# Performance work log

Hardware: AMD Instinct MI355X
Metric: run time of the kernel (lower is better)

## Reference

```python
import jax, jax.numpy as jnp
import numpy as np

N_NODES = 100000
N_EDGES = 1600000
IN_DIM = 512
OUT_DIM = 64


def setup_inputs() -> dict:
    key = jax.random.key(0)
    k1, k2, k3 = jax.random.split(key, 3)
    x = jax.random.normal(k1, (N_NODES, IN_DIM), dtype=jnp.float32)
    edge_index = jax.random.randint(k2, (2, N_EDGES), 0, N_NODES, dtype=jnp.int64)
    # Glorot-ish init for the GCNConv linear weight, stored as [in, out]
    W = jax.random.normal(k3, (IN_DIM, OUT_DIM), dtype=jnp.float32) * (1.0 / np.sqrt(IN_DIM))
    b = jnp.zeros((OUT_DIM,), dtype=jnp.float32)
    return {"x": x, "edge_index": edge_index, "W": W, "b": b}


def reference(x, edge_index, W, b):
    N = x.shape[0]
    # --- gcn_norm: add self-loops, symmetric degree normalization ---
    loop = jnp.arange(N, dtype=edge_index.dtype)
    src = jnp.concatenate([edge_index[0], loop])  # message sources
    dst = jnp.concatenate([edge_index[1], loop])  # aggregation targets
    deg = jax.ops.segment_sum(jnp.ones_like(dst, dtype=x.dtype), dst, num_segments=N)
    deg_inv_sqrt = jnp.where(deg > 0, jax.lax.rsqrt(jnp.maximum(deg, 1.0)), 0.0)
    norm = deg_inv_sqrt[src] * deg_inv_sqrt[dst]  # [E+N]
    # --- linear transform then gather-scale-scatter aggregation ---
    h = x @ W                                   # [N, out]
    msg = h[src] * norm[:, None]                # [E+N, out]
    out = jax.ops.segment_sum(msg, dst, num_segments=N) + b
    return jax.nn.log_softmax(out, axis=1)
```

## Files before the change

### kernel.cpp

```cpp
#include <hip/hip_runtime.h>
#include <math.h>

#define N_NODES 100000
#define N_EDGES 1600000
#define IN_DIM 512
#define OUT_DIM 64
#define NB 1024
#define NPB 128
#define CHUNK (N_EDGES / NPB)
#define N_BUCKETS_USED 782
#define N_TILES128 782
#define GEMM_BLOCKS 256

typedef __attribute__((ext_vector_type(8))) short short8;
typedef __attribute__((ext_vector_type(4))) float float4v;

__device__ __forceinline__ unsigned short f2bf(float f) {
    unsigned int u = __float_as_uint(f);
    u += 0x7fffu + ((u >> 16) & 1u);
    return (unsigned short)(u >> 16);
}
__device__ __forceinline__ float bf2f(unsigned short s) {
    return __uint_as_float(((unsigned int)s) << 16);
}
__device__ __forceinline__ short8 cvt8(float4v lo, float4v hi) {
    union { short8 s8; unsigned short us[8]; } af;
    af.us[0] = f2bf(lo.x); af.us[1] = f2bf(lo.y);
    af.us[2] = f2bf(lo.z); af.us[3] = f2bf(lo.w);
    af.us[4] = f2bf(hi.x); af.us[5] = f2bf(hi.y);
    af.us[6] = f2bf(hi.z); af.us[7] = f2bf(hi.w);
    return af.s8;
}
__device__ __forceinline__ void gload_lds16(const void* g, void* lds) {
    __builtin_amdgcn_global_load_lds(
        (const __attribute__((address_space(1))) unsigned int*)g,
        (__attribute__((address_space(3))) unsigned int*)lds, 16, 0, 0);
}

__global__ __launch_bounds__(256) void k_hist1(const int* __restrict__ dst,
                                               int* __restrict__ blockHist) {
    __shared__ int hist[NB];
    const int t = threadIdx.x, b = blockIdx.x;
    for (int k = t; k < NB; k += 256) hist[k] = 0;
    __syncthreads();
    const int e0 = b * CHUNK;
    for (int i = t; i < CHUNK; i += 256)
        atomicAdd(&hist[dst[e0 + i] >> 7], 1);
    __syncthreads();
    for (int k = t; k < NB; k += 256) blockHist[k * NPB + b] = hist[k];
}

__global__ __launch_bounds__(256) void k_offsets(const int* __restrict__ blockHist,
                                                 int* __restrict__ blockStart,
                                                 int* __restrict__ bucketBase) {
    __shared__ int colsum[NB];
    __shared__ int bbase[NB + 1];
    __shared__ int wtot[4];
    const int t = threadIdx.x, lane = t & 63, w = t >> 6;
    for (int k = t; k < NB; k += 256) {
        const int4* p = (const int4*)(blockHist + k * NPB);
        int s = 0;
#pragma unroll
        for (int j = 0; j < NPB / 4; ++j) {
            int4 v = p[j];
            s += v.x + v.y + v.z + v.w;
        }
        colsum[k] = s;
    }
    __syncthreads();
    int c0 = colsum[t * 4 + 0], c1 = colsum[t * 4 + 1];
    int c2 = colsum[t * 4 + 2], c3 = colsum[t * 4 + 3];
    int tsum = c0 + c1 + c2 + c3;
    int incl = tsum;
#pragma unroll
    for (int off = 1; off < 64; off <<= 1) {
        int u = __shfl_up(incl, off, 64);
        if (lane >= off) incl += u;
    }
    if (lane == 63) wtot[w] = incl;
    __syncthreads();
    int woff = 0;
#pragma unroll
    for (int k2 = 0; k2 < 4; ++k2) if (k2 < w) woff += wtot[k2];
    int excl = woff + incl - tsum;
    bbase[t * 4 + 0] = excl;
    bbase[t * 4 + 1] = excl + c0;
    bbase[t * 4 + 2] = excl + c0 + c1;
    bbase[t * 4 + 3] = excl + c0 + c1 + c2;
    if (t == 255) bbase[NB] = excl + tsum;
    __syncthreads();
    for (int k = t; k < NB + 1; k += 256) bucketBase[k] = bbase[k];
    for (int k = t; k < NB; k += 256) {
        int run = bbase[k];
        const int* ph = blockHist + k * NPB;
        int* ps = blockStart + k * NPB;
        for (int b = 0; b < NPB; ++b) {
            ps[b] = run;
            run += ph[b];
        }
    }
}

__global__ __launch_bounds__(256) void k_partition(const int* __restrict__ dst,
                                                   const int* __restrict__ src,
                                                   const int* __restrict__ blockStart,
                                                   int* __restrict__ parts) {
    __shared__ int cursor[NB];
    const int t = threadIdx.x, b = blockIdx.x;
    for (int k = t; k < NB; k += 256) cursor[k] = blockStart[k * NPB + b];
    __syncthreads();
    const int e0 = b * CHUNK;
    for (int i = t; i < CHUNK; i += 256) {
        int d = dst[e0 + i];
        int s = src[e0 + i];
        int k = d >> 7;
        int pos = atomicAdd(&cursor[k], 1);
        parts[pos] = ((d & 127) << 17) | s;
    }
}

__global__ __launch_bounds__(256) void k_bucket(const int* __restrict__ parts,
                                                const int* __restrict__ bucketBase,
                                                int* __restrict__ degi,
                                                int* __restrict__ row_ptr,
                                                int* __restrict__ csr) {
    __shared__ int cnt[128];
    __shared__ int cur[128];
    __shared__ int wtot[2];
    const int t = threadIdx.x, k = blockIdx.x;
    const int base = bucketBase[k];
    const int n    = bucketBase[k + 1] - base;
    if (t < 128) cnt[t] = 0;
    __syncthreads();
    for (int i = t; i < n; i += 256)
        atomicAdd(&cnt[parts[base + i] >> 17], 1);
    __syncthreads();
    int incl = 0, v = 0;
    if (t < 128) {
        int lane = t & 63;
        v = cnt[t];
        incl = v;
#pragma unroll
        for (int off = 1; off < 64; off <<= 1) {
            int u = __shfl_up(incl, off, 64);
            if (lane >= off) incl += u;
        }
        if (lane == 63) wtot[t >> 6] = incl;
    }
    __syncthreads();
    if (t < 128) {
        int excl = incl - v + ((t >> 6) ? wtot[0] : 0);
        cur[t] = excl;
        int node = k * 128 + t;
        if (node < N_NODES) {
            degi[node]    = v;
            row_ptr[node] = base + excl;
        }
    }
    __syncthreads();
    for (int i = t; i < n; i += 256) {
        int code = parts[base + i];
        int nl = code >> 17, s = code & 0x1FFFF;
        int pos = atomicAdd(&cur[nl], 1);
        csr[base + pos] = s;
    }
}

__global__ __launch_bounds__(256) void k_wswz(const float* __restrict__ W,
                                              unsigned short* __restrict__ Wswz) {
    int t = blockIdx.x * 256 + threadIdx.x;
    if (t < IN_DIM * OUT_DIM) {
        int k = t >> 6, n = t & 63;
        int kt = k >> 5, kin = k & 31;
        int quad = kin >> 3, j = kin & 7;
        int ct = n >> 4, l16 = n & 15;
        int lane = quad * 16 + l16;
        Wswz[(((kt * 4 + ct) * 64 + lane) * 8) + j] = f2bf(W[t]);
    }
}

__global__ __launch_bounds__(512) void k_gemm(const float* __restrict__ x,
                                              const unsigned short* __restrict__ Wswz,
                                              const int* __restrict__ degi,
                                              unsigned short* __restrict__ h) {
    __shared__ short8 Wlds[64][64];
    __shared__ float  xbuf[2][8192];
    const int t = threadIdx.x;
    {
        const float4v* s = (const float4v*)Wswz;
        float4v* d = (float4v*)Wlds;
        for (int i = t; i < 4096; i += 512) d[i] = s[i];
    }

    const int lane = t & 63;
    const int w    = t >> 6;
    const int quad = lane >> 4, l16 = lane & 15;

    int p0[4], prow[4], pwin[4];
#pragma unroll
    for (int c = 0; c < 4; ++c) {
        int p = (w * 4 + c) * 1024 + lane * 16;
        p0[c] = p;
        int r = p >> 8;
        prow[c] = r;
        pwin[c] = (p & 255) ^ ((r & 7) << 4);
    }

    auto STAGE = [&](int rowBase, int s, int buf) {
#pragma unroll
        for (int c = 0; c < 4; ++c) {
            int rg = rowBase + prow[c];
            rg = rg < N_NODES ? rg : (N_NODES - 1);
            const float* g = x + (size_t)rg * IN_DIM + s * 64 + (pwin[c] >> 2);
            char* lp = ((char*)xbuf) + buf * 32768 + p0[c];
            gload_lds16(g, lp);
        }
    };

    const int rl   = w * 16 + l16;
    const int sw   = (rl & 7) << 4;
    const int rb   = rl * 256;

    int tile = blockIdx.x;
    STAGE(tile * 128, 0, 0);
    __syncthreads();

    while (true) {
        const int rowBase = tile * 128;
        float4v acc[4] = {{0.f,0.f,0.f,0.f},{0.f,0.f,0.f,0.f},
                          {0.f,0.f,0.f,0.f},{0.f,0.f,0.f,0.f}};
#pragma unroll 1
        for (int s = 0; s < 8; ++s) {
            if (s < 7) {
                STAGE(rowBase, s + 1, (s + 1) & 1);
            } else {
                int nt = tile + GEMM_BLOCKS;
                if (nt < N_TILES128) STAGE(nt * 128, 0, 0);
            }
            const char* Xb = ((const char*)xbuf) + (s & 1) * 32768;
#pragma unroll
            for (int kt = 0; kt < 2; ++kt) {
                int boff = rb + ((kt * 128 + quad * 32) ^ sw);
                float4v lo = *(const float4v*)(Xb + boff);
                float4v hi = *(const float4v*)(Xb + (boff ^ 16));
                short8 a = cvt8(lo, hi);
#pragma unroll
                for (int ct = 0; ct < 4; ++ct) {
                    short8 bf = Wlds[(s * 2 + kt) * 4 + ct][lane];
                    acc[ct] = __builtin_amdgcn_mfma_f32_16x16x32_bf16(a, bf, acc[ct], 0, 0, 0);
                }
            }
            __syncthreads();
        }
#pragma unroll
        for (int reg = 0; reg < 4; ++reg) {
            int orow = rowBase + w * 16 + quad * 4 + reg;
            if (orow < N_NODES) {
                float dinv = rsqrtf((float)(degi[orow] + 1));
#pragma unroll
                for (int ct = 0; ct < 4; ++ct)
                    h[(size_t)orow * OUT_DIM + ct * 16 + l16] = f2bf(acc[ct][reg] * dinv);
            }
        }
        tile += GEMM_BLOCKS;
        if (tile >= N_TILES128) break;
    }
}

__global__ __launch_bounds__(256) void k_gather(const int* __restrict__ degi,
                                                const int* __restrict__ row_ptr,
                                                const int* __restrict__ csr,
                                                const unsigned short* __restrict__ h,
                                                const float* __restrict__ b,
                                                float* __restrict__ out) {
    int node = blockIdx.x * 4 + (threadIdx.x >> 6);
    int lane = threadIdx.x & 63;
    if (node >= N_NODES) return;
    int cnt  = __builtin_amdgcn_readfirstlane(degi[node]);
    int base = __builtin_amdgcn_readfirstlane(row_ptr[node]);

    float acc = bf2f(h[(size_t)node * OUT_DIM + lane]);
    int e = 0;
    for (; e + 8 <= cnt; e += 8) {
        int s0 = csr[base + e + 0], s1 = csr[base + e + 1];
        int s2 = csr[base + e + 2], s3 = csr[base + e + 3];
        int s4 = csr[base + e + 4], s5 = csr[base + e + 5];
        int s6 = csr[base + e + 6], s7 = csr[base + e + 7];
        float v0 = bf2f(h[(size_t)s0 * OUT_DIM + lane]);
        float v1 = bf2f(h[(size_t)s1 * OUT_DIM + lane]);
        float v2 = bf2f(h[(size_t)s2 * OUT_DIM + lane]);
        float v3 = bf2f(h[(size_t)s3 * OUT_DIM + lane]);
        float v4 = bf2f(h[(size_t)s4 * OUT_DIM + lane]);
        float v5 = bf2f(h[(size_t)s5 * OUT_DIM + lane]);
        float v6 = bf2f(h[(size_t)s6 * OUT_DIM + lane]);
        float v7 = bf2f(h[(size_t)s7 * OUT_DIM + lane]);
        acc += ((v0 + v1) + (v2 + v3)) + ((v4 + v5) + (v6 + v7));
    }
    for (; e < cnt; ++e)
        acc += bf2f(h[(size_t)csr[base + e] * OUT_DIM + lane]);

    float v = acc * rsqrtf((float)(cnt + 1)) + b[lane];
    float m = v;
#pragma unroll
    for (int off = 32; off > 0; off >>= 1) m = fmaxf(m, __shfl_xor(m, off, 64));
    float ex = expf(v - m);
    float s = ex;
#pragma unroll
    for (int off = 32; off > 0; off >>= 1) s += __shfl_xor(s, off, 64);
    out[(size_t)node * OUT_DIM + lane] = v - m - logf(s);
}

extern "C" void kernel_launch(void* const* d_in, const int* in_sizes, int n_in,
                              void* d_out, int out_size, void* d_ws, size_t ws_size,
                              hipStream_t stream) {
    const float* x  = (const float*)d_in[0];
    const int*   ei = (const int*)d_in[1];
    const float* W  = (const float*)d_in[2];
    const float* b  = (const float*)d_in[3];
    float* out = (float*)d_out;

    char* ws = (char*)d_ws;
    int*            degi       = (int*)(ws + 0);
    int*            row_ptr    = (int*)(ws + 400000);
    int*            blockHist  = (int*)(ws + 800000);
    int*            blockStart = (int*)(ws + 1324288);
    int*            bucketBase = (int*)(ws + 1848576);
    unsigned short* Wswz       = (unsigned short*)(ws + 1852928);
    unsigned short* h          = (unsigned short*)(ws + 1918464);
    int*            parts      = (int*)(ws + 14718464);
    int*            csr        = (int*)(ws + 21118464);

    const int* src = ei;
    const int* dst = ei + N_EDGES;

    k_hist1    <<<NPB, 256, 0, stream>>>(dst, blockHist);
    k_offsets  <<<1,   256, 0, stream>>>(blockHist, blockStart, bucketBase);
    k_partition<<<NPB, 256, 0, stream>>>(dst, src, blockStart, parts);
    k_bucket   <<<N_BUCKETS_USED, 256, 0, stream>>>(parts, bucketBase, degi, row_ptr, csr);
    k_wswz     <<<(IN_DIM * OUT_DIM + 255) / 256, 256, 0, stream>>>(W, Wswz);
    k_gemm     <<<GEMM_BLOCKS, 512, 0, stream>>>(x, Wswz, degi, h);
    k_gather   <<<(N_NODES + 3) / 4, 256, 0, stream>>>(degi, row_ptr, csr, h, b, out);
}
```

Baseline: 478.9 us.

## Flatten GEMM tile/k-step loops into one pipelined stage loop with explicit waitcnt

Merges the per-tile and per-k-slice loops of the x@W GEMM into a single flattened stage loop, so prefetching of the next slice continues across tile boundaries. It replaces __syncthreads with explicit s_waitcnt vmcnt(4)/lgkmcnt(0) plus raw s_barrier, so only the older load group is waited on while the newly issued prefetch stays in flight. The aim is to hide global-to-LDS latency better. The hand-tuned waitcnt counts are fragile and depend on exactly four loads being issued per stage.

```diff
diff --git a/kernel.cpp b/kernel.cpp
--- a/kernel.cpp
+++ b/kernel.cpp
@@ -206,13 +206,19 @@
         pwin[c] = (p & 255) ^ ((r & 7) << 4);
     }
 
-    auto STAGE = [&](int rowBase, int s, int buf) {
+    const int ntiles = (blockIdx.x < (N_TILES128 - (N_TILES128 / GEMM_BLOCKS) * GEMM_BLOCKS))
+                         ? (N_TILES128 / GEMM_BLOCKS + 1) : (N_TILES128 / GEMM_BLOCKS);
+    const int F = ntiles * 8;
+
+    auto STAGEF = [&](int f) {
+        int rowBase = (blockIdx.x + (f >> 3) * GEMM_BLOCKS) * 128;
+        int s = f & 7;
 #pragma unroll
         for (int c = 0; c < 4; ++c) {
             int rg = rowBase + prow[c];
             rg = rg < N_NODES ? rg : (N_NODES - 1);
             const float* g = x + (size_t)rg * IN_DIM + s * 64 + (pwin[c] >> 2);
-            char* lp = ((char*)xbuf) + buf * 32768 + p0[c];
+            char* lp = ((char*)xbuf) + (f & 1) * 32768 + p0[c];
             gload_lds16(g, lp);
         }
     };
@@ -221,49 +227,58 @@
     const int sw   = (rl & 7) << 4;
     const int rb   = rl * 256;
 
-    int tile = blockIdx.x;
-    STAGE(tile * 128, 0, 0);
-    __syncthreads();
-
-    while (true) {
-        const int rowBase = tile * 128;
-        float4v acc[4] = {{0.f,0.f,0.f,0.f},{0.f,0.f,0.f,0.f},
-                          {0.f,0.f,0.f,0.f},{0.f,0.f,0.f,0.f}};
+    __syncthreads();
+    STAGEF(0);
+
+    float4v acc[4] = {{0.f,0.f,0.f,0.f},{0.f,0.f,0.f,0.f},
+                      {0.f,0.f,0.f,0.f},{0.f,0.f,0.f,0.f}};
+
 #pragma unroll 1
-        for (int s = 0; s < 8; ++s) {
-            if (s < 7) {
-                STAGE(rowBase, s + 1, (s + 1) & 1);
-            } else {
-                int nt = tile + GEMM_BLOCKS;
-                if (nt < N_TILES128) STAGE(nt * 128, 0, 0);
+    for (int f = 0; f < F; ++f) {
+        if (f + 1 < F) {
+            STAGEF(f + 1);
+            asm volatile("s_waitcnt vmcnt(4)" ::: "memory");
+        } else {
+            asm volatile("s_waitcnt vmcnt(0)" ::: "memory");
+        }
+        __builtin_amdgcn_sched_barrier(0);
+        __builtin_amdgcn_s_barrier();
+
+        const int s = f & 7;
+        const char* Xb = ((const char*)xbuf) + (f & 1) * 32768;
+#pragma unroll
+        for (int kt = 0; kt < 2; ++kt) {
+            int boff = rb + ((kt * 128 + quad * 32) ^ sw);
+            float4v lo = *(const float4v*)(Xb + boff);
+            float4v hi = *(const float4v*)(Xb + (boff ^ 16));
+            short8 a = cvt8(lo, hi);
+#pragma unroll
+            for (int ct = 0; ct < 4; ++ct) {
+                short8 bf = Wlds[(s * 2 + kt) * 4 + ct][lane];
+                acc[ct] = __builtin_amdgcn_mfma_f32_16x16x32_bf16(a, bf, acc[ct], 0, 0, 0);
             }
-            const char* Xb = ((const char*)xbuf) + (s & 1) * 32768;
-#pragma unroll
-            for (int kt = 0; kt < 2; ++kt) {
-                int boff = rb + ((kt * 128 + quad * 32) ^ sw);
-                float4v lo = *(const float4v*)(Xb + boff);
-                float4v hi = *(const float4v*)(Xb + (boff ^ 16));
-                short8 a = cvt8(lo, hi);
-#pragma unroll
-                for (int ct = 0; ct < 4; ++ct) {
-                    short8 bf = Wlds[(s * 2 + kt) * 4 + ct][lane];
-                    acc[ct] = __builtin_amdgcn_mfma_f32_16x16x32_bf16(a, bf, acc[ct], 0, 0, 0);
+        }
+
+        if (s == 7) {
+            int rowBase = (blockIdx.x + (f >> 3) * GEMM_BLOCKS) * 128;
+#pragma unroll
+            for (int reg = 0; reg < 4; ++reg) {
+                int orow = rowBase + w * 16 + quad * 4 + reg;
+                if (orow < N_NODES) {
+                    float dinv = rsqrtf((float)(degi[orow] + 1));
+#pragma unroll
+                    for (int ct = 0; ct < 4; ++ct)
+                        h[(size_t)orow * OUT_DIM + ct * 16 + l16] = f2bf(acc[ct][reg] * dinv);
                 }
             }
-            __syncthreads();
-        }
-#pragma unroll
-        for (int reg = 0; reg < 4; ++reg) {
-            int orow = rowBase + w * 16 + quad * 4 + reg;
-            if (orow < N_NODES) {
-                float dinv = rsqrtf((float)(degi[orow] + 1));
-#pragma unroll
-                for (int ct = 0; ct < 4; ++ct)
-                    h[(size_t)orow * OUT_DIM + ct * 16 + l16] = f2bf(acc[ct][reg] * dinv);
-            }
-        }
-        tile += GEMM_BLOCKS;
-        if (tile >= N_TILES128) break;
+#pragma unroll
+            for (int ct = 0; ct < 4; ++ct)
+                acc[ct] = (float4v){0.f, 0.f, 0.f, 0.f};
+        }
+
+        asm volatile("s_waitcnt lgkmcnt(0)" ::: "memory");
+        __builtin_amdgcn_sched_barrier(0);
+        __builtin_amdgcn_s_barrier();
     }
 }
 
```

Result: no change. 481.7 us (+0.6%).
